# Performance work log

Hardware: AMD Instinct MI355X
Metric: run time of the kernel (lower is better)

The kernel has to match this reference:

```python
import jax, jax.numpy as jnp
import numpy as np

K = 2  # num_experts_used (top-k)


def setup_inputs() -> dict:
    key = jax.random.key(0)
    ks = jax.random.split(key, 6)
    B, S, D, U, E = 2, 2048, 1024, 4096, 8
    return {
        "x": jax.random.normal(ks[0], (B, S, D), dtype=jnp.float32),
        "w_router": jax.random.normal(ks[1], (E, D), dtype=jnp.float32),
        "w_up": jax.random.normal(ks[2], (E, U, D), dtype=jnp.float32),
        "b_up": jax.random.normal(ks[3], (E, U), dtype=jnp.float32),
        "w_down": jax.random.normal(ks[4], (E, D, U), dtype=jnp.float32),
        "b_down": jax.random.normal(ks[5], (E, D), dtype=jnp.float32),
    }


def reference(x, w_router, w_up, b_up, w_down, b_down):
    # Router: Linear(embed_dim -> num_experts), no bias
    logits = jnp.einsum('bsd,ed->bse', x, w_router)
    top_logits, idx = jax.lax.top_k(logits, K)          # [b,s,k]
    router_weights = jax.nn.softmax(top_logits, axis=-1)  # softmax over top-k logits

    # Compute all-expert FFN outputs (same math as per-token gathered weights,
    # without materializing the (b,s,k,u,d) weight copies of the original).
    h = jnp.einsum('eud,bsd->bseu', w_up, x) + b_up[None, None]   # [b,s,E,u]
    h = jax.nn.gelu(h, approximate=False)
    y = jnp.einsum('edu,bseu->bsed', w_down, h) + b_down[None, None]  # [b,s,E,d]

    # Gather outputs of the top-k experts per token
    y_k = jnp.take_along_axis(y, idx[..., None], axis=2)  # [b,s,k,d]
    out = jnp.einsum('bskd,bsk->bsd', y_k, router_weights)
    return out
```

## Files before the change

### kernel.cpp

```cpp
#include <hip/hip_runtime.h>
#include <hip/hip_bf16.h>
#include <stdint.h>
#include <math.h>

#define TTOK 4096
#define DDIM 1024
#define UDIM 4096
#define NEXP 8
#define KSPLIT 2
#define KCH   (UDIM / KSPLIT)
#define NPAIR (TTOK * 2)
#define EPAD 72

using float4v = __attribute__((ext_vector_type(4))) float;
using short8  = __attribute__((ext_vector_type(8))) short;
using ushort8 = __attribute__((ext_vector_type(8))) unsigned short;

__device__ __forceinline__ unsigned short f2bf(float f) {
  union { float f; unsigned u; } v; v.f = f;
  unsigned r = v.u + 0x7FFFu + ((v.u >> 16) & 1u);
  return (unsigned short)(r >> 16);
}
__device__ __forceinline__ float bf2f(unsigned short u) {
  union { unsigned u; float f; } v; v.u = ((unsigned)u) << 16;
  return v.f;
}
__device__ __forceinline__ void load_lds16(const void* g, void* l) {
  __builtin_amdgcn_global_load_lds(
      (const __attribute__((address_space(1))) unsigned int*)g,
      (__attribute__((address_space(3))) unsigned int*)l, 16, 0, 0);
}
__device__ __forceinline__ short8 cvt8(const float4v a, const float4v b) {
  union { __hip_bfloat162 h[4]; short8 s; } u;
  u.h[0] = __float22bfloat162_rn(make_float2(a[0], a[1]));
  u.h[1] = __float22bfloat162_rn(make_float2(a[2], a[3]));
  u.h[2] = __float22bfloat162_rn(make_float2(b[0], b[1]));
  u.h[3] = __float22bfloat162_rn(make_float2(b[2], b[3]));
  return u.s;
}
__device__ __forceinline__ float gelu_f(float v) {
  float u = v * (0.7978845608f + 0.0356774081f * v * v);
  float ex = __expf(2.0f * u);
  return v * (1.0f - 1.0f / (1.0f + ex));
}

__device__ __forceinline__ void router_body(
    int t, int lane, const float* __restrict__ x, const float* __restrict__ wr,
    int* __restrict__ counts, int* __restrict__ list,
    float* __restrict__ wpair, int* __restrict__ epair,
    unsigned short* __restrict__ xb) {
  float acc[NEXP];
#pragma unroll
  for (int e = 0; e < NEXP; e++) acc[e] = 0.0f;
  const float* xr = x + (size_t)t * DDIM;
  unsigned short* xbr = xb + (size_t)t * DDIM;
  for (int d = lane; d < DDIM; d += 64) {
    float xv = xr[d];
    xbr[d] = f2bf(xv);
#pragma unroll
    for (int e = 0; e < NEXP; e++) acc[e] += xv * wr[e * DDIM + d];
  }
#pragma unroll
  for (int e = 0; e < NEXP; e++) {
#pragma unroll
    for (int off = 32; off > 0; off >>= 1) acc[e] += __shfl_xor(acc[e], off, 64);
  }
  if (lane == 0) {
    int e0 = 0; float l0 = acc[0];
    for (int e = 1; e < NEXP; e++) if (acc[e] > l0) { l0 = acc[e]; e0 = e; }
    int e1 = -1; float l1 = -3.4e38f;
    for (int e = 0; e < NEXP; e++) if (e != e0 && acc[e] > l1) { l1 = acc[e]; e1 = e; }
    float s1 = expf(l1 - l0);
    float inv = 1.0f / (1.0f + s1);
    int p0 = atomicAdd(&counts[e0], 1);
    list[e0 * TTOK + p0] = 2 * t;
    wpair[2 * t] = inv;  epair[2 * t] = e0;
    int p1 = atomicAdd(&counts[e1], 1);
    list[e1 * TTOK + p1] = 2 * t + 1;
    wpair[2 * t + 1] = s1 * inv;  epair[2 * t + 1] = e1;
  }
}

__global__ void router_kernel(const float* __restrict__ x,
                              const float* __restrict__ wr,
                              int* __restrict__ counts, int* __restrict__ list,
                              float* __restrict__ wpair, int* __restrict__ epair,
                              unsigned short* __restrict__ xb) {
  const int t = blockIdx.x * 4 + (threadIdx.x >> 6);
  router_body(t, threadIdx.x & 63, x, wr, counts, list, wpair, epair, xb);
}

__global__ void prep_kernel(const float* __restrict__ x, const float* __restrict__ wr,
                            int* __restrict__ counts, int* __restrict__ list,
                            float* __restrict__ wpair, int* __restrict__ epair,
                            unsigned short* __restrict__ xb,
                            const float* __restrict__ wu, const float* __restrict__ wd,
                            unsigned short* __restrict__ wub, unsigned short* __restrict__ wdb) {
  const int bid = blockIdx.x;
  if (bid < TTOK / 4) {
    const int t = bid * 4 + (threadIdx.x >> 6);
    router_body(t, threadIdx.x & 63, x, wr, counts, list, wpair, epair, xb);
    return;
  }
  const size_t n8 = (size_t)NEXP * UDIM * DDIM / 8;
  const size_t cb = (size_t)(bid - TTOK / 4);
  const size_t stride = (size_t)(gridDim.x - TTOK / 4) * 256;
  for (size_t i = cb * 256 + threadIdx.x; i < 2 * n8; i += stride) {
    const float* s; unsigned short* d;
    if (i < n8) { s = wu + i * 8; d = wub + i * 8; }
    else        { s = wd + (i - n8) * 8; d = wdb + (i - n8) * 8; }
    float4v lo = *(const float4v*)s;
    float4v hi = *(const float4v*)(s + 4);
    short8 v = cvt8(lo, hi);
    *(short8*)d = v;
  }
}

__global__ __launch_bounds__(256, 4) void stage_up_b16(
    const unsigned short* __restrict__ xb, const unsigned short* __restrict__ wub,
    const float* __restrict__ bup, const int* __restrict__ counts,
    const int* __restrict__ list, unsigned short* __restrict__ h) {
  const int e = blockIdx.z, mt = blockIdx.y, nt = blockIdx.x;
  const int cnt = counts[e];
  if (mt * 128 >= cnt) return;
  const int rem = min(128, cnt - mt * 128);
  const int* lst = list + e * TTOK + mt * 128;

  __shared__ __align__(16) char SM[18432];
  unsigned short* Sb = (unsigned short*)SM;

  const int tid = threadIdx.x;
  const int wave = tid >> 6, lane = tid & 63;
  const int srow = tid >> 2, cell = tid & 3;

  const int tok0 = lst[min(srow, rem - 1)] >> 1;
  const int tok1 = lst[min(srow + 64, rem - 1)] >> 1;
  const unsigned short* a0 = xb + (size_t)tok0 * DDIM + cell * 8;
  const unsigned short* a1 = xb + (size_t)tok1 * DDIM + cell * 8;
  const unsigned short* b0 = wub + ((size_t)e * UDIM + nt * 128 + srow) * DDIM + cell * 8;
  const unsigned short* b1 = b0 + (size_t)64 * DDIM;

  const int wm = wave >> 1, wn = wave & 1;
  const int lane15 = lane & 15, quad = lane >> 4;
  const int abyte = (wm * 64 + lane15) * 64 + quad * 16;
  const int bbyte = 8192 + (wn * 64 + lane15) * 64 + quad * 16;

  float4v acc[4][4];
#pragma unroll
  for (int i = 0; i < 4; i++)
#pragma unroll
    for (int j = 0; j < 4; j++) acc[i][j] = (float4v){0.f, 0.f, 0.f, 0.f};

  for (int k0 = 0; k0 < DDIM; k0 += 32) {
    load_lds16(a0 + k0, SM + tid * 16);
    load_lds16(a1 + k0, SM + 4096 + tid * 16);
    load_lds16(b0 + k0, SM + 8192 + tid * 16);
    load_lds16(b1 + k0, SM + 12288 + tid * 16);
    __syncthreads();
    short8 af[4], bfr[4];
#pragma unroll
    for (int mi = 0; mi < 4; mi++) af[mi] = *(const short8*)(SM + abyte + mi * 1024);
#pragma unroll
    for (int ni = 0; ni < 4; ni++) bfr[ni] = *(const short8*)(SM + bbyte + ni * 1024);
#pragma unroll
    for (int mi = 0; mi < 4; mi++)
#pragma unroll
      for (int ni = 0; ni < 4; ni++)
        acc[mi][ni] = __builtin_amdgcn_mfma_f32_16x16x32_bf16(af[mi], bfr[ni], acc[mi][ni], 0, 0, 0);
    __syncthreads();
  }

  const int ucol0 = nt * 128 + wn * 64;
  float bias[4];
#pragma unroll
  for (int ni = 0; ni < 4; ni++) bias[ni] = bup[e * UDIM + ucol0 + ni * 16 + lane15];
  const int row = tid >> 1, seg = tid & 1;
  const int opair = (row < rem) ? lst[row] : -1;
#pragma unroll
  for (int hh = 0; hh < 2; hh++) {
    if (wn == hh) {
#pragma unroll
      for (int mi = 0; mi < 4; mi++)
#pragma unroll
        for (int r = 0; r < 4; r++) {
          const int rl = wm * 64 + mi * 16 + quad * 4 + r;
#pragma unroll
          for (int ni = 0; ni < 4; ni++)
            Sb[rl * EPAD + ni * 16 + lane15] = f2bf(gelu_f(acc[mi][ni][r] + bias[ni]));
        }
    }
    __syncthreads();
    if (opair >= 0) {
      unsigned short* dst = h + (size_t)opair * UDIM + nt * 128 + hh * 64 + seg * 32;
      const unsigned short* src = Sb + row * EPAD + seg * 32;
#pragma unroll
      for (int c = 0; c < 4; c++) *(ushort8*)(dst + c * 8) = *(const ushort8*)(src + c * 8);
    }
    __syncthreads();
  }
}

__global__ __launch_bounds__(256, 4) void stage_down_b16(
    const unsigned short* __restrict__ h, const unsigned short* __restrict__ wdb,
    const int* __restrict__ counts, const int* __restrict__ list,
    unsigned short* __restrict__ part) {
  const int e = blockIdx.z, mt = blockIdx.y >> 1, kc = blockIdx.y & 1, nt = blockIdx.x;
  const int cnt = counts[e];
  if (mt * 128 >= cnt) return;
  const int rem = min(128, cnt - mt * 128);
  const int* lst = list + e * TTOK + mt * 128;

  __shared__ __align__(16) char SM[18432];
  unsigned short* Sb = (unsigned short*)SM;

  const int tid = threadIdx.x;
  const int wave = tid >> 6, lane = tid & 63;
  const int srow = tid >> 2, cell = tid & 3;

  const int pr0 = lst[min(srow, rem - 1)];
  const int pr1 = lst[min(srow + 64, rem - 1)];
  const unsigned short* a0 = h + (size_t)pr0 * UDIM + kc * KCH + cell * 8;
  const unsigned short* a1 = h + (size_t)pr1 * UDIM + kc * KCH + cell * 8;
  const unsigned short* b0 = wdb + ((size_t)e * DDIM + nt * 128 + srow) * UDIM + kc * KCH + cell * 8;
  const unsigned short* b1 = b0 + (size_t)64 * UDIM;

  const int wm = wave >> 1, wn = wave & 1;
  const int lane15 = lane & 15, quad = lane >> 4;
  const int abyte = (wm * 64 + lane15) * 64 + quad * 16;
  const int bbyte = 8192 + (wn * 64 + lane15) * 64 + quad * 16;

  float4v acc[4][4];
#pragma unroll
  for (int i = 0; i < 4; i++)
#pragma unroll
    for (int j = 0; j < 4; j++) acc[i][j] = (float4v){0.f, 0.f, 0.f, 0.f};

  for (int k0 = 0; k0 < KCH; k0 += 32) {
    load_lds16(a0 + k0, SM + tid * 16);
    load_lds16(a1 + k0, SM + 4096 + tid * 16);
    load_lds16(b0 + k0, SM + 8192 + tid * 16);
    load_lds16(b1 + k0, SM + 12288 + tid * 16);
    __syncthreads();
    short8 af[4], bfr[4];
#pragma unroll
    for (int mi = 0; mi < 4; mi++) af[mi] = *(const short8*)(SM + abyte + mi * 1024);
#pragma unroll
    for (int ni = 0; ni < 4; ni++) bfr[ni] = *(const short8*)(SM + bbyte + ni * 1024);
#pragma unroll
    for (int mi = 0; mi < 4; mi++)
#pragma unroll
      for (int ni = 0; ni < 4; ni++)
        acc[mi][ni] = __builtin_amdgcn_mfma_f32_16x16x32_bf16(af[mi], bfr[ni], acc[mi][ni], 0, 0, 0);
    __syncthreads();
  }

  const int row = tid >> 1, seg = tid & 1;
  const int opair = (row < rem) ? lst[row] : -1;
#pragma unroll
  for (int hh = 0; hh < 2; hh++) {
    if (wn == hh) {
#pragma unroll
      for (int mi = 0; mi < 4; mi++)
#pragma unroll
        for (int r = 0; r < 4; r++) {
          const int rl = wm * 64 + mi * 16 + quad * 4 + r;
#pragma unroll
          for (int ni = 0; ni < 4; ni++)
            Sb[rl * EPAD + ni * 16 + lane15] = f2bf(acc[mi][ni][r]);
        }
    }
    __syncthreads();
    if (opair >= 0) {
      unsigned short* dst = part + ((size_t)kc * NPAIR + opair) * DDIM + nt * 128 + hh * 64 + seg * 32;
      const unsigned short* src = Sb + row * EPAD + seg * 32;
#pragma unroll
      for (int c = 0; c < 4; c++) *(ushort8*)(dst + c * 8) = *(const ushort8*)(src + c * 8);
    }
    __syncthreads();
  }
}

__global__ __launch_bounds__(256, 3) void stage_up_k(
    const unsigned short* __restrict__ xb, const float* __restrict__ wu,
    const float* __restrict__ bup, const int* __restrict__ counts,
    const int* __restrict__ list, unsigned short* __restrict__ h) {
  const int e = blockIdx.z, mt = blockIdx.y, nt = blockIdx.x;
  const int cnt = counts[e];
  if (mt * 128 >= cnt) return;
  const int rem = min(128, cnt - mt * 128);
  const int* lst = list + e * TTOK + mt * 128;

  __shared__ __align__(16) char SM[24576];
  unsigned short* Sb = (unsigned short*)SM;

  const int tid = threadIdx.x;
  const int wave = tid >> 6, lane = tid & 63;
  const int srow = tid >> 2, cell = tid & 3;
  const int brow = tid >> 3;
  const int bswz = (tid & 7) ^ (brow & 7);

  const int tok0 = lst[min(srow, rem - 1)] >> 1;
  const int tok1 = lst[min(srow + 64, rem - 1)] >> 1;
  const unsigned short* a0 = xb + (size_t)tok0 * DDIM + cell * 8;
  const unsigned short* a1 = xb + (size_t)tok1 * DDIM + cell * 8;
  const float* bbase = wu + ((size_t)e * UDIM + nt * 128) * DDIM;
  const float* bsrc[4];
#pragma unroll
  for (int k = 0; k < 4; k++) bsrc[k] = bbase + (size_t)(brow + k * 32) * DDIM + bswz * 4;

  const int wm = wave >> 1, wn = wave & 1;
  const int lane15 = lane & 15, quad = lane >> 4;
  const int abyte = (wm * 64 + lane15) * 64 + quad * 16;
  const int p0 = (2 * quad) ^ (lane & 7);
  const int bbyte = 8192 + (wn * 64 + lane15) * 128;

  float4v acc[4][4];
#pragma unroll
  for (int i = 0; i < 4; i++)
#pragma unroll
    for (int j = 0; j < 4; j++) acc[i][j] = (float4v){0.f, 0.f, 0.f, 0.f};

  for (int k0 = 0; k0 < DDIM; k0 += 32) {
    load_lds16(a0 + k0, SM + tid * 16);
    load_lds16(a1 + k0, SM + 4096 + tid * 16);
#pragma unroll
    for (int k = 0; k < 4; k++) load_lds16(bsrc[k] + k0, SM + 8192 + k * 4096 + tid * 16);
    __syncthreads();
    short8 af[4], bfr[4];
#pragma unroll
    for (int mi = 0; mi < 4; mi++) af[mi] = *(const short8*)(SM + abyte + mi * 1024);
#pragma unroll
    for (int ni = 0; ni < 4; ni++) {
      const char* rb = SM + bbyte + ni * 2048;
      float4v f0 = *(const float4v*)(rb + p0 * 16);
      float4v f1 = *(const float4v*)(rb + (p0 ^ 1) * 16);
      bfr[ni] = cvt8(f0, f1);
    }
#pragma unroll
    for (int mi = 0; mi < 4; mi++)
#pragma unroll
      for (int ni = 0; ni < 4; ni++)
        acc[mi][ni] = __builtin_amdgcn_mfma_f32_16x16x32_bf16(af[mi], bfr[ni], acc[mi][ni], 0, 0, 0);
    __syncthreads();
  }

  const int ucol0 = nt * 128 + wn * 64;
  float bias[4];
#pragma unroll
  for (int ni = 0; ni < 4; ni++) bias[ni] = bup[e * UDIM + ucol0 + ni * 16 + lane15];
  const int row = tid >> 1, seg = tid & 1;
  const int opair = (row < rem) ? lst[row] : -1;
#pragma unroll
  for (int hh = 0; hh < 2; hh++) {
    if (wn == hh) {
#pragma unroll
      for (int mi = 0; mi < 4; mi++)
#pragma unroll
        for (int r = 0; r < 4; r++) {
          const int rl = wm * 64 + mi * 16 + quad * 4 + r;
#pragma unroll
          for (int ni = 0; ni < 4; ni++)
            Sb[rl * EPAD + ni * 16 + lane15] = f2bf(gelu_f(acc[mi][ni][r] + bias[ni]));
        }
    }
    __syncthreads();
    if (opair >= 0) {
      unsigned short* dst = h + (size_t)opair * UDIM + nt * 128 + hh * 64 + seg * 32;
      const unsigned short* src = Sb + row * EPAD + seg * 32;
#pragma unroll
      for (int c = 0; c < 4; c++) *(ushort8*)(dst + c * 8) = *(const ushort8*)(src + c * 8);
    }
    __syncthreads();
  }
}

template <bool PARTM>
__global__ __launch_bounds__(256, 3) void stage_down_k(
    const unsigned short* __restrict__ h, const float* __restrict__ wd,
    const float* __restrict__ bdn, const float* __restrict__ wpair,
    const int* __restrict__ counts, const int* __restrict__ list,
    unsigned short* __restrict__ part, float* __restrict__ out) {
  const int e = blockIdx.z, mt = blockIdx.y >> 1, kc = blockIdx.y & 1, nt = blockIdx.x;
  const int cnt = counts[e];
  if (mt * 128 >= cnt) return;
  const int rem = min(128, cnt - mt * 128);
  const int* lst = list + e * TTOK + mt * 128;

  __shared__ __align__(16) char SM[24576];
  unsigned short* Sb = (unsigned short*)SM;

  const int tid = threadIdx.x;
  const int wave = tid >> 6, lane = tid & 63;
  const int srow = tid >> 2, cell = tid & 3;
  const int brow = tid >> 3;
  const int bswz = (tid & 7) ^ (brow & 7);

  const int pr0 = lst[min(srow, rem - 1)];
  const int pr1 = lst[min(srow + 64, rem - 1)];
  const unsigned short* a0 = h + (size_t)pr0 * UDIM + kc * KCH + cell * 8;
  const unsigned short* a1 = h + (size_t)pr1 * UDIM + kc * KCH + cell * 8;
  const float* bbase = wd + ((size_t)e * DDIM + nt * 128) * UDIM + kc * KCH;
  const float* bsrc[4];
#pragma unroll
  for (int k = 0; k < 4; k++) bsrc[k] = bbase + (size_t)(brow + k * 32) * UDIM + bswz * 4;

  const int wm = wave >> 1, wn = wave & 1;
  const int lane15 = lane & 15, quad = lane >> 4;
  const int abyte = (wm * 64 + lane15) * 64 + quad * 16;
  const int p0 = (2 * quad) ^ (lane & 7);
  const int bbyte = 8192 + (wn * 64 + lane15) * 128;

  float4v acc[4][4];
#pragma unroll
  for (int i = 0; i < 4; i++)
#pragma unroll
    for (int j = 0; j < 4; j++) acc[i][j] = (float4v){0.f, 0.f, 0.f, 0.f};

  for (int k0 = 0; k0 < KCH; k0 += 32) {
    load_lds16(a0 + k0, SM + tid * 16);
    load_lds16(a1 + k0, SM + 4096 + tid * 16);
#pragma unroll
    for (int k = 0; k < 4; k++) load_lds16(bsrc[k] + k0, SM + 8192 + k * 4096 + tid * 16);
    __syncthreads();
    short8 af[4], bfr[4];
#pragma unroll
    for (int mi = 0; mi < 4; mi++) af[mi] = *(const short8*)(SM + abyte + mi * 1024);
#pragma unroll
    for (int ni = 0; ni < 4; ni++) {
      const char* rb = SM + bbyte + ni * 2048;
      float4v f0 = *(const float4v*)(rb + p0 * 16);
      float4v f1 = *(const float4v*)(rb + (p0 ^ 1) * 16);
      bfr[ni] = cvt8(f0, f1);
    }
#pragma unroll
    for (int mi = 0; mi < 4; mi++)
#pragma unroll
      for (int ni = 0; ni < 4; ni++)
        acc[mi][ni] = __builtin_amdgcn_mfma_f32_16x16x32_bf16(af[mi], bfr[ni], acc[mi][ni], 0, 0, 0);
    __syncthreads();
  }

  const int dcol0 = nt * 128 + wn * 64;
  if constexpr (PARTM) {
    const int row = tid >> 1, seg = tid & 1;
    const int opair = (row < rem) ? lst[row] : -1;
#pragma unroll
    for (int hh = 0; hh < 2; hh++) {
      if (wn == hh) {
#pragma unroll
        for (int mi = 0; mi < 4; mi++)
#pragma unroll
          for (int r = 0; r < 4; r++) {
            const int rl = wm * 64 + mi * 16 + quad * 4 + r;
#pragma unroll
            for (int ni = 0; ni < 4; ni++)
              Sb[rl * EPAD + ni * 16 + lane15] = f2bf(acc[mi][ni][r]);
          }
      }
      __syncthreads();
      if (opair >= 0) {
        unsigned short* dst = part + ((size_t)kc * NPAIR + opair) * DDIM + nt * 128 + hh * 64 + seg * 32;
        const unsigned short* src = Sb + row * EPAD + seg * 32;
#pragma unroll
        for (int c = 0; c < 4; c++) *(ushort8*)(dst + c * 8) = *(const ushort8*)(src + c * 8);
      }
      __syncthreads();
    }
  } else {
    float bias[4];
#pragma unroll
    for (int ni = 0; ni < 4; ni++)
      bias[ni] = (kc == 0) ? bdn[e * DDIM + dcol0 + ni * 16 + lane15] : 0.0f;
#pragma unroll
    for (int mi = 0; mi < 4; mi++)
#pragma unroll
      for (int r = 0; r < 4; r++) {
        const int mrow = wm * 64 + mi * 16 + quad * 4 + r;
        if (mrow < rem) {
          const int pair = lst[mrow];
          const float w = wpair[pair];
          float* orow = out + (size_t)(pair >> 1) * DDIM;
#pragma unroll
          for (int ni = 0; ni < 4; ni++)
            atomicAdd(&orow[dcol0 + ni * 16 + lane15], w * (acc[mi][ni][r] + bias[ni]));
        }
      }
  }
}

__global__ void combine_kernel(const unsigned short* __restrict__ part,
                               const float* __restrict__ bdn,
                               const float* __restrict__ wpair,
                               const int* __restrict__ epair,
                               float* __restrict__ out) {
  const int idx = blockIdx.x * 256 + threadIdx.x;
  const int t = idx >> 7, c8 = (idx & 127) * 8;
  const size_t kstride = (size_t)NPAIR * DDIM;
  const unsigned short* pa = part + (size_t)(2 * t) * DDIM + c8;
  float s0[8], s1[8];
#pragma unroll
  for (int j = 0; j < 8; j++) { s0[j] = 0.f; s1[j] = 0.f; }
#pragma unroll
  for (int kc = 0; kc < KSPLIT; kc++) {
    ushort8 a = *(const ushort8*)(pa + kc * kstride);
    ushort8 b = *(const ushort8*)(pa + kc * kstride + DDIM);
#pragma unroll
    for (int j = 0; j < 8; j++) { s0[j] += bf2f(a[j]); s1[j] += bf2f(b[j]); }
  }
  const float w0 = wpair[2 * t], w1 = wpair[2 * t + 1];
  const int e0 = epair[2 * t], e1 = epair[2 * t + 1];
  const float* b0 = bdn + e0 * DDIM + c8;
  const float* b1 = bdn + e1 * DDIM + c8;
  float4v o[2];
#pragma unroll
  for (int half = 0; half < 2; half++)
#pragma unroll
    for (int j = 0; j < 4; j++) {
      const int jj = half * 4 + j;
      o[half][j] = w0 * (s0[jj] + b0[jj]) + w1 * (s1[jj] + b1[jj]);
    }
  float4v* dst = (float4v*)(out + (size_t)t * DDIM + c8);
  dst[0] = o[0]; dst[1] = o[1];
}

__global__ void zero_out_k(float4v* __restrict__ out) {
  const int tid = blockIdx.x * blockDim.x + threadIdx.x;
  const int O4 = TTOK * DDIM / 4;
  const int stride = gridDim.x * blockDim.x;
  for (int i = tid; i < O4; i += stride) out[i] = (float4v){0.f, 0.f, 0.f, 0.f};
}

extern "C" void kernel_launch(void* const* d_in, const int* in_sizes, int n_in,
                              void* d_out, int out_size, void* d_ws, size_t ws_size,
                              hipStream_t stream) {
  (void)in_sizes; (void)n_in; (void)out_size;
  const float* x        = (const float*)d_in[0];
  const float* w_router = (const float*)d_in[1];
  const float* w_up     = (const float*)d_in[2];
  const float* b_up     = (const float*)d_in[3];
  const float* w_down   = (const float*)d_in[4];
  const float* b_down   = (const float*)d_in[5];
  float* out = (float*)d_out;

  char* ws = (char*)d_ws;
  size_t off = 0;
  auto take = [&](size_t b) { size_t o = off; off = (off + b + 255) & ~(size_t)255; return o; };
  unsigned short* h  = (unsigned short*)(ws + take((size_t)NPAIR * UDIM * 2));
  unsigned short* xb = (unsigned short*)(ws + take((size_t)TTOK * DDIM * 2));
  int* counts        = (int*)(ws + take(NEXP * 4));
  int* list          = (int*)(ws + take((size_t)NEXP * TTOK * 4));
  float* wpair       = (float*)(ws + take((size_t)NPAIR * 4));
  int* epair         = (int*)(ws + take((size_t)NPAIR * 4));
  size_t part_off    = take((size_t)KSPLIT * NPAIR * DDIM * 2);
  const bool partmode = ws_size >= off;
  size_t wub_off     = take((size_t)NEXP * UDIM * DDIM * 2);
  size_t wdb_off     = take((size_t)NEXP * DDIM * UDIM * 2);
  const bool bf16mode = ws_size >= off;

  hipMemsetAsync(counts, 0, NEXP * 4, stream);

  if (bf16mode) {
    unsigned short* part = (unsigned short*)(ws + part_off);
    unsigned short* wub  = (unsigned short*)(ws + wub_off);
    unsigned short* wdb  = (unsigned short*)(ws + wdb_off);
    prep_kernel<<<TTOK / 4 + 2048, 256, 0, stream>>>(
        x, w_router, counts, list, wpair, epair, xb, w_up, w_down, wub, wdb);
    stage_up_b16<<<dim3(UDIM / 128, 32, NEXP), 256, 0, stream>>>(
        xb, wub, b_up, counts, list, h);
    stage_down_b16<<<dim3(DDIM / 128, 32 * KSPLIT, NEXP), 256, 0, stream>>>(
        h, wdb, counts, list, part);
    combine_kernel<<<TTOK * DDIM / 8 / 256, 256, 0, stream>>>(part, b_down, wpair, epair, out);
  } else {
    router_kernel<<<TTOK / 4, 256, 0, stream>>>(x, w_router, counts, list, wpair, epair, xb);
    stage_up_k<<<dim3(UDIM / 128, 32, NEXP), 256, 0, stream>>>(xb, w_up, b_up, counts, list, h);
    if (partmode) {
      unsigned short* part = (unsigned short*)(ws + part_off);
      stage_down_k<true><<<dim3(DDIM / 128, 32 * KSPLIT, NEXP), 256, 0, stream>>>(
          h, w_down, b_down, wpair, counts, list, part, out);
      combine_kernel<<<TTOK * DDIM / 8 / 256, 256, 0, stream>>>(part, b_down, wpair, epair, out);
    } else {
      zero_out_k<<<1024, 256, 0, stream>>>((float4v*)out);
      stage_down_k<false><<<dim3(DDIM / 128, 32 * KSPLIT, NEXP), 256, 0, stream>>>(
          h, w_down, b_down, wpair, counts, list, (unsigned short*)nullptr, out);
    }
  }
}
```

Before: 651.9 us.

## Batch router atomics per block, pad expert counters, and restructure weight conversion

The router in prep_kernel now handles 32 tokens per block using vectorized float4 loads. Each block tallies its per-expert assignments in LDS and issues one atomicAdd per expert instead of one per token pair. Expert counters are padded to separate cache lines to reduce atomic contention. The weight fp32-to-bf16 conversion switches from a grid-stride loop to fixed 4096-element chunks per block. In exchange, list ordering becomes block-grouped, and the router part has fewer blocks, which may lengthen its critical path.

```diff
diff --git a/kernel.cpp b/kernel.cpp
--- a/kernel.cpp
+++ b/kernel.cpp
@@ -11,10 +11,14 @@
 #define KCH   (UDIM / KSPLIT)
 #define NPAIR (TTOK * 2)
 #define EPAD 72
+#define CPAD 32
+#define RBLK 128
+#define CBLK 2048
 
 using float4v = __attribute__((ext_vector_type(4))) float;
 using short8  = __attribute__((ext_vector_type(8))) short;
 using ushort8 = __attribute__((ext_vector_type(8))) unsigned short;
+using ushort4v = __attribute__((ext_vector_type(4))) unsigned short;
 
 __device__ __forceinline__ unsigned short f2bf(float f) {
   union { float f; unsigned u; } v; v.f = f;
@@ -44,11 +48,13 @@
   return v * (1.0f - 1.0f / (1.0f + ex));
 }
 
-__device__ __forceinline__ void router_body(
-    int t, int lane, const float* __restrict__ x, const float* __restrict__ wr,
-    int* __restrict__ counts, int* __restrict__ list,
-    float* __restrict__ wpair, int* __restrict__ epair,
-    unsigned short* __restrict__ xb) {
+__global__ void router_kernel(const float* __restrict__ x,
+                              const float* __restrict__ wr,
+                              int* __restrict__ counts, int* __restrict__ list,
+                              float* __restrict__ wpair, int* __restrict__ epair,
+                              unsigned short* __restrict__ xb) {
+  const int t = blockIdx.x * 4 + (threadIdx.x >> 6);
+  const int lane = threadIdx.x & 63;
   float acc[NEXP];
 #pragma unroll
   for (int e = 0; e < NEXP; e++) acc[e] = 0.0f;
@@ -72,22 +78,13 @@
     for (int e = 0; e < NEXP; e++) if (e != e0 && acc[e] > l1) { l1 = acc[e]; e1 = e; }
     float s1 = expf(l1 - l0);
     float inv = 1.0f / (1.0f + s1);
-    int p0 = atomicAdd(&counts[e0], 1);
+    int p0 = atomicAdd(&counts[e0 * CPAD], 1);
     list[e0 * TTOK + p0] = 2 * t;
     wpair[2 * t] = inv;  epair[2 * t] = e0;
-    int p1 = atomicAdd(&counts[e1], 1);
+    int p1 = atomicAdd(&counts[e1 * CPAD], 1);
     list[e1 * TTOK + p1] = 2 * t + 1;
     wpair[2 * t + 1] = s1 * inv;  epair[2 * t + 1] = e1;
   }
-}
-
-__global__ void router_kernel(const float* __restrict__ x,
-                              const float* __restrict__ wr,
-                              int* __restrict__ counts, int* __restrict__ list,
-                              float* __restrict__ wpair, int* __restrict__ epair,
-                              unsigned short* __restrict__ xb) {
-  const int t = blockIdx.x * 4 + (threadIdx.x >> 6);
-  router_body(t, threadIdx.x & 63, x, wr, counts, list, wpair, epair, xb);
 }
 
 __global__ void prep_kernel(const float* __restrict__ x, const float* __restrict__ wr,
@@ -96,23 +93,81 @@
                             unsigned short* __restrict__ xb,
                             const float* __restrict__ wu, const float* __restrict__ wd,
                             unsigned short* __restrict__ wub, unsigned short* __restrict__ wdb) {
+  __shared__ int sE0[32], sE1[32];
   const int bid = blockIdx.x;
-  if (bid < TTOK / 4) {
-    const int t = bid * 4 + (threadIdx.x >> 6);
-    router_body(t, threadIdx.x & 63, x, wr, counts, list, wpair, epair, xb);
+  const int tid = threadIdx.x;
+
+  if (bid < RBLK) {
+    const int wave = tid >> 6, lane = tid & 63;
+#pragma unroll 1
+    for (int j = 0; j < 8; j++) {
+      const int slot = wave * 8 + j;
+      const int t = bid * 32 + slot;
+      float acc[NEXP];
+#pragma unroll
+      for (int e = 0; e < NEXP; e++) acc[e] = 0.0f;
+      const float* xr = x + (size_t)t * DDIM;
+      unsigned short* xbr = xb + (size_t)t * DDIM;
+#pragma unroll
+      for (int it = 0; it < 4; it++) {
+        const int d = it * 256 + lane * 4;
+        float4v xv = *(const float4v*)(xr + d);
+        ushort4v xo;
+#pragma unroll
+        for (int c = 0; c < 4; c++) xo[c] = f2bf(xv[c]);
+        *(ushort4v*)(xbr + d) = xo;
+#pragma unroll
+        for (int e = 0; e < NEXP; e++) {
+          float4v wv = *(const float4v*)(wr + e * DDIM + d);
+          acc[e] += xv[0] * wv[0] + xv[1] * wv[1] + xv[2] * wv[2] + xv[3] * wv[3];
+        }
+      }
+#pragma unroll
+      for (int e = 0; e < NEXP; e++) {
+#pragma unroll
+        for (int off = 32; off > 0; off >>= 1) acc[e] += __shfl_xor(acc[e], off, 64);
+      }
+      if (lane == 0) {
+        int e0 = 0; float l0 = acc[0];
+        for (int e = 1; e < NEXP; e++) if (acc[e] > l0) { l0 = acc[e]; e0 = e; }
+        int e1 = -1; float l1 = -3.4e38f;
+        for (int e = 0; e < NEXP; e++) if (e != e0 && acc[e] > l1) { l1 = acc[e]; e1 = e; }
+        float s1 = expf(l1 - l0);
+        float inv = 1.0f / (1.0f + s1);
+        wpair[2 * t] = inv;          epair[2 * t] = e0;
+        wpair[2 * t + 1] = s1 * inv; epair[2 * t + 1] = e1;
+        sE0[slot] = e0;  sE1[slot] = e1;
+      }
+    }
+    __syncthreads();
+    if (tid < NEXP) {
+      const int e = tid;
+      int cnt = 0;
+#pragma unroll
+      for (int s = 0; s < 32; s++) cnt += (sE0[s] == e) + (sE1[s] == e);
+      int r = atomicAdd(&counts[e * CPAD], cnt);
+      int* le = list + e * TTOK;
+#pragma unroll 1
+      for (int s = 0; s < 32; s++) {
+        const int p = 2 * (bid * 32 + s);
+        if (sE0[s] == e) le[r++] = p;
+        if (sE1[s] == e) le[r++] = p + 1;
+      }
+    }
     return;
   }
-  const size_t n8 = (size_t)NEXP * UDIM * DDIM / 8;
-  const size_t cb = (size_t)(bid - TTOK / 4);
-  const size_t stride = (size_t)(gridDim.x - TTOK / 4) * 256;
-  for (size_t i = cb * 256 + threadIdx.x; i < 2 * n8; i += stride) {
-    const float* s; unsigned short* d;
-    if (i < n8) { s = wu + i * 8; d = wub + i * 8; }
-    else        { s = wd + (i - n8) * 8; d = wdb + (i - n8) * 8; }
-    float4v lo = *(const float4v*)s;
-    float4v hi = *(const float4v*)(s + 4);
-    short8 v = cvt8(lo, hi);
-    *(short8*)d = v;
+
+  const int cb = bid - RBLK;
+  const float* s; unsigned short* d;
+  size_t i0;
+  if (cb < CBLK / 2) { s = wu; d = wub; i0 = (size_t)cb * 4096; }
+  else               { s = wd; d = wdb; i0 = (size_t)(cb - CBLK / 2) * 4096; }
+#pragma unroll
+  for (int it = 0; it < 16; it++) {
+    const size_t i = i0 + (size_t)it * 256 + tid;
+    float4v lo = *(const float4v*)(s + i * 8);
+    float4v hi = *(const float4v*)(s + i * 8 + 4);
+    *(short8*)(d + i * 8) = cvt8(lo, hi);
   }
 }
 
@@ -121,7 +176,7 @@
     const float* __restrict__ bup, const int* __restrict__ counts,
     const int* __restrict__ list, unsigned short* __restrict__ h) {
   const int e = blockIdx.z, mt = blockIdx.y, nt = blockIdx.x;
-  const int cnt = counts[e];
+  const int cnt = counts[e * CPAD];
   if (mt * 128 >= cnt) return;
   const int rem = min(128, cnt - mt * 128);
   const int* lst = list + e * TTOK + mt * 128;
@@ -205,7 +260,7 @@
     const int* __restrict__ counts, const int* __restrict__ list,
     unsigned short* __restrict__ part) {
   const int e = blockIdx.z, mt = blockIdx.y >> 1, kc = blockIdx.y & 1, nt = blockIdx.x;
-  const int cnt = counts[e];
+  const int cnt = counts[e * CPAD];
   if (mt * 128 >= cnt) return;
   const int rem = min(128, cnt - mt * 128);
   const int* lst = list + e * TTOK + mt * 128;
@@ -285,7 +340,7 @@
     const float* __restrict__ bup, const int* __restrict__ counts,
     const int* __restrict__ list, unsigned short* __restrict__ h) {
   const int e = blockIdx.z, mt = blockIdx.y, nt = blockIdx.x;
-  const int cnt = counts[e];
+  const int cnt = counts[e * CPAD];
   if (mt * 128 >= cnt) return;
   const int rem = min(128, cnt - mt * 128);
   const int* lst = list + e * TTOK + mt * 128;
@@ -381,7 +436,7 @@
     const int* __restrict__ counts, const int* __restrict__ list,
     unsigned short* __restrict__ part, float* __restrict__ out) {
   const int e = blockIdx.z, mt = blockIdx.y >> 1, kc = blockIdx.y & 1, nt = blockIdx.x;
-  const int cnt = counts[e];
+  const int cnt = counts[e * CPAD];
   if (mt * 128 >= cnt) return;
   const int rem = min(128, cnt - mt * 128);
   const int* lst = list + e * TTOK + mt * 128;
@@ -547,7 +602,7 @@
   auto take = [&](size_t b) { size_t o = off; off = (off + b + 255) & ~(size_t)255; return o; };
   unsigned short* h  = (unsigned short*)(ws + take((size_t)NPAIR * UDIM * 2));
   unsigned short* xb = (unsigned short*)(ws + take((size_t)TTOK * DDIM * 2));
-  int* counts        = (int*)(ws + take(NEXP * 4));
+  int* counts        = (int*)(ws + take(NEXP * CPAD * 4));
   int* list          = (int*)(ws + take((size_t)NEXP * TTOK * 4));
   float* wpair       = (float*)(ws + take((size_t)NPAIR * 4));
   int* epair         = (int*)(ws + take((size_t)NPAIR * 4));
@@ -557,13 +612,13 @@
   size_t wdb_off     = take((size_t)NEXP * DDIM * UDIM * 2);
   const bool bf16mode = ws_size >= off;
 
-  hipMemsetAsync(counts, 0, NEXP * 4, stream);
+  hipMemsetAsync(counts, 0, NEXP * CPAD * 4, stream);
 
   if (bf16mode) {
     unsigned short* part = (unsigned short*)(ws + part_off);
     unsigned short* wub  = (unsigned short*)(ws + wub_off);
     unsigned short* wdb  = (unsigned short*)(ws + wdb_off);
-    prep_kernel<<<TTOK / 4 + 2048, 256, 0, stream>>>(
+    prep_kernel<<<RBLK + CBLK, 256, 0, stream>>>(
         x, w_router, counts, list, wpair, epair, xb, w_up, w_down, wub, wdb);
     stage_up_b16<<<dim3(UDIM / 128, 32, NEXP), 256, 0, stream>>>(
         xb, wub, b_up, counts, list, h);
```

After: 602.9 us. 7.5% less time.
